# Kernel tuning notes

Measured on AMD Instinct MI355X. Metric: run time of the kernel, lower is better.

## Reference

```python
import jax, jax.numpy as jnp
import numpy as np

MARGIN = 0.2
SCALE = 30.0

def setup_inputs() -> dict:
    key = jax.random.key(0)
    k1, k2 = jax.random.split(key)
    B, D, C = 8192, 512, 100
    embeddings = jax.random.normal(k1, (B, D), dtype=jnp.float32)
    labels = jax.random.randint(k2, (B,), 0, C, dtype=jnp.int64)
    return {"embeddings": embeddings, "labels": labels}

def reference(embeddings, labels):
    # Cosine similarity via one GEMM: normalize rows once, then n @ n.T.
    # (torch F.cosine_similarity uses eps=1e-8 on norms)
    norms = jnp.maximum(jnp.linalg.norm(embeddings, axis=1, keepdims=True), 1e-8)
    n = embeddings / norms                      # [B, D]
    sim = n @ n.T                               # [B, B]
    pos_mask = labels[:, None] == labels[None, :]  # includes diagonal, as in original
    e = jnp.exp(SCALE * (sim - MARGIN))         # [B, B]
    pos_sum = jnp.sum(jnp.where(pos_mask, e, 0.0))
    neg_sum = jnp.sum(jnp.where(pos_mask, 0.0, e))
    loss = jnp.log1p(neg_sum / pos_sum)
    return loss
```

## Files before the change

kernel.cpp:

```cpp
#include <hip/hip_runtime.h>
#include <hip/hip_bf16.h>
#include <math.h>


#define BDIM 8192
#define DDIM 512
#define MARGIN 0.2f
#define SCALE 30.0f

#define BT 256
#define BK 64
#define NKT (DDIM / BK)
#define NT (BDIM / BT)
#define NBLK (NT * (NT + 1) / 2)

typedef __hip_bfloat16 bf16;
using f32x4  = __attribute__((ext_vector_type(4))) float;
using bf16x8 = __attribute__((ext_vector_type(8))) short;
using us8    = __attribute__((ext_vector_type(8))) unsigned short;

#define GLOAD_LDS16(gp, lp)                                                    \
    __builtin_amdgcn_global_load_lds(                                          \
        (const __attribute__((address_space(1))) unsigned int*)(gp),           \
        (__attribute__((address_space(3))) unsigned int*)(lp), 16, 0, 0)

__device__ __forceinline__ unsigned short f2bf(float x) {
    union { bf16 h; unsigned short u; } c;
    c.h = __float2bfloat16(x);
    return c.u;
}

__global__ __launch_bounds__(256)
void norm_rows_kernel(const float* __restrict__ emb, bf16* __restrict__ nout,
                      double* __restrict__ accum, unsigned* __restrict__ ctr) {
    if (blockIdx.x == 0 && threadIdx.x == 0) {
        accum[0] = 0.0; accum[1] = 0.0; *ctr = 0u;
    }
    const int row  = blockIdx.x * 4 + (threadIdx.x >> 6);
    const int lane = threadIdx.x & 63;
    const float4* src = (const float4*)(emb + (size_t)row * DDIM) + lane * 2;
    const float4 a = src[0];
    const float4 b = src[1];
    float ss = a.x * a.x + a.y * a.y + a.z * a.z + a.w * a.w
             + b.x * b.x + b.y * b.y + b.z * b.z + b.w * b.w;
    #pragma unroll
    for (int off = 1; off < 64; off <<= 1) ss += __shfl_xor(ss, off, 64);
    const float inv = 1.0f / fmaxf(sqrtf(ss), 1e-8f);
    float v[8] = { a.x, a.y, a.z, a.w, b.x, b.y, b.z, b.w };
    us8 o;
    #pragma unroll
    for (int i = 0; i < 8; ++i) o[i] = f2bf(v[i] * inv);
    *((us8*)(nout + (size_t)row * DDIM) + lane) = o;
}

__global__ __launch_bounds__(512, 2)
void gemm_loss_kernel(const bf16* __restrict__ nmat,
                      const int* __restrict__ labels,
                      double* __restrict__ accum, unsigned* __restrict__ ctr,
                      float* __restrict__ out) {
    const int l = blockIdx.x;
    auto tri = [](int b) { return ((65 - b) * b) >> 1; };
    int bi = (int)((65.0 - sqrt(4225.0 - 8.0 * (double)l)) * 0.5);
    bi = bi < 0 ? 0 : (bi > 31 ? 31 : bi);
    while (bi > 0 && tri(bi) > l) --bi;
    while (tri(bi + 1) <= l) ++bi;
    const int bj = bi + (l - tri(bi));

    __shared__ short As[2][BT * BK];
    __shared__ short Bs[2][BT * BK];
    __shared__ int lr[BT], lc[BT];
    __shared__ double red[16];

    const int t = threadIdx.x, wid = t >> 6, lane = t & 63;
    if (t < 256) lr[t] = labels[bi * BT + t];
    else         lc[t - 256] = labels[bj * BT + (t - 256)];

    const int wm = wid >> 2;
    const int wn = wid & 3;

    const int srow = wid * 16 + (lane >> 3);
    const int swz8 = ((lane & 7) ^ (lane >> 3)) * 8;
    const bf16* gA = nmat + (size_t)(bi * BT + srow) * DDIM + swz8;
    const bf16* gB = nmat + (size_t)(bj * BT + srow) * DDIM + swz8;
    const int ldsw = wid * 1024;

    #define STAGE_A(buf, kt, h)                                                 \
        do {                                                                    \
            GLOAD_LDS16(gA + (size_t)(h) * 128 * DDIM + (kt) * BK,              \
                        &As[buf][(h) * 8192 + ldsw]);                           \
            GLOAD_LDS16(gA + (size_t)(h) * 128 * DDIM + 8 * DDIM + (kt) * BK,   \
                        &As[buf][(h) * 8192 + ldsw + 512]);                     \
        } while (0)
    #define STAGE_B(buf, kt, h)                                                 \
        do {                                                                    \
            GLOAD_LDS16(gB + (size_t)(h) * 128 * DDIM + (kt) * BK,              \
                        &Bs[buf][(h) * 8192 + ldsw]);                           \
            GLOAD_LDS16(gB + (size_t)(h) * 128 * DDIM + 8 * DDIM + (kt) * BK,   \
                        &Bs[buf][(h) * 8192 + ldsw + 512]);                     \
        } while (0)

    const int arow = (wm * 128 + (lane & 15)) * BK;
    const int brow = (wn * 64 + (lane & 15)) * BK;
    const int chk0 = (((lane >> 4) + 0) ^ (lane & 7)) * 8;
    const int chk1 = (((lane >> 4) + 4) ^ (lane & 7)) * 8;

    f32x4 acc[8][4] = {};

    STAGE_A(0, 0, 0); STAGE_A(0, 0, 1); STAGE_B(0, 0, 0); STAGE_B(0, 0, 1);

    #pragma unroll 2
    for (int kt = 0; kt < NKT; ++kt) {
        const int cur = kt & 1, nxt = cur ^ 1;
        const bool more = (kt + 1 < NKT);
        if (more) {
            STAGE_A(nxt, kt + 1, 0);
            asm volatile("s_waitcnt vmcnt(2)" ::: "memory");
        } else {
            asm volatile("s_waitcnt vmcnt(0)" ::: "memory");
        }
        __builtin_amdgcn_s_barrier();
        asm volatile("" ::: "memory");

        bf16x8 a[4], b[4], a2[4];
        #pragma unroll
        for (int m = 0; m < 4; ++m)
            a[m] = *(const bf16x8*)&As[cur][arow + m * 1024 + chk0];
        #pragma unroll
        for (int n = 0; n < 4; ++n)
            b[n] = *(const bf16x8*)&Bs[cur][brow + n * 1024 + chk0];
        if (more) STAGE_A(nxt, kt + 1, 1);
        __builtin_amdgcn_s_setprio(1);
        #pragma unroll
        for (int m = 0; m < 4; ++m)
            #pragma unroll
            for (int n = 0; n < 4; ++n)
                acc[m][n] = __builtin_amdgcn_mfma_f32_16x16x32_bf16(
                    a[m], b[n], acc[m][n], 0, 0, 0);
        __builtin_amdgcn_s_setprio(0);
        #pragma unroll
        for (int m = 0; m < 4; ++m)
            a2[m] = *(const bf16x8*)&As[cur][arow + (m + 4) * 1024 + chk0];
        if (more) STAGE_B(nxt, kt + 1, 0);
        __builtin_amdgcn_s_setprio(1);
        #pragma unroll
        for (int m = 0; m < 4; ++m)
            #pragma unroll
            for (int n = 0; n < 4; ++n)
                acc[m + 4][n] = __builtin_amdgcn_mfma_f32_16x16x32_bf16(
                    a2[m], b[n], acc[m + 4][n], 0, 0, 0);
        __builtin_amdgcn_s_setprio(0);
        #pragma unroll
        for (int m = 0; m < 4; ++m)
            a[m] = *(const bf16x8*)&As[cur][arow + m * 1024 + chk1];
        #pragma unroll
        for (int n = 0; n < 4; ++n)
            b[n] = *(const bf16x8*)&Bs[cur][brow + n * 1024 + chk1];
        if (more) STAGE_B(nxt, kt + 1, 1);
        __builtin_amdgcn_s_setprio(1);
        #pragma unroll
        for (int m = 0; m < 4; ++m)
            #pragma unroll
            for (int n = 0; n < 4; ++n)
                acc[m][n] = __builtin_amdgcn_mfma_f32_16x16x32_bf16(
                    a[m], b[n], acc[m][n], 0, 0, 0);
        __builtin_amdgcn_s_setprio(0);
        #pragma unroll
        for (int m = 0; m < 4; ++m)
            a2[m] = *(const bf16x8*)&As[cur][arow + (m + 4) * 1024 + chk1];
        asm volatile("s_waitcnt lgkmcnt(0)" ::: "memory");
        __builtin_amdgcn_sched_barrier(0);
        __builtin_amdgcn_s_barrier();
        asm volatile("" ::: "memory");
        __builtin_amdgcn_s_setprio(1);
        #pragma unroll
        for (int m = 0; m < 4; ++m)
            #pragma unroll
            for (int n = 0; n < 4; ++n)
                acc[m + 4][n] = __builtin_amdgcn_mfma_f32_16x16x32_bf16(
                    a2[m], b[n], acc[m + 4][n], 0, 0, 0);
        __builtin_amdgcn_s_setprio(0);
    }
    #undef STAGE_A
    #undef STAGE_B

    float posf = 0.0f, negf = 0.0f;
    const int rbase = wm * 128 + (lane >> 4) * 4;
    const int cbase = wn * 64 + (lane & 15);
    #pragma unroll
    for (int m = 0; m < 8; ++m) {
        #pragma unroll
        for (int n = 0; n < 4; ++n) {
            const int ljv = lc[cbase + n * 16];
            #pragma unroll
            for (int r = 0; r < 4; ++r) {
                const float e = __expf(fmaf(acc[m][n][r], SCALE, -SCALE * MARGIN));
                if (lr[rbase + m * 16 + r] == ljv) posf += e; else negf += e;
            }
        }
    }

    double dp = (double)posf, dn = (double)negf;
    #pragma unroll
    for (int o = 32; o > 0; o >>= 1) {
        dp += __shfl_down(dp, o, 64);
        dn += __shfl_down(dn, o, 64);
    }
    if (lane == 0) { red[wid * 2] = dp; red[wid * 2 + 1] = dn; }
    __syncthreads();
    if (t == 0) {
        const double w = (bi == bj) ? 1.0 : 2.0;
        double p = 0.0, q = 0.0;
        #pragma unroll
        for (int i = 0; i < 8; ++i) { p += red[2 * i]; q += red[2 * i + 1]; }
        atomicAdd(&accum[0], p * w);
        atomicAdd(&accum[1], q * w);
        __threadfence();
        unsigned prev = atomicAdd(ctr, 1u);
        if (prev == NBLK - 1) {
            __threadfence();
            double pp = atomicAdd(&accum[0], 0.0);
            double qq = atomicAdd(&accum[1], 0.0);
            out[0] = (float)log1p(qq / pp);
        }
    }
}

extern "C" void kernel_launch(void* const* d_in, const int* in_sizes, int n_in,
                              void* d_out, int out_size, void* d_ws, size_t ws_size,
                              hipStream_t stream) {
    const float* emb  = (const float*)d_in[0];
    const int* labels = (const int*)d_in[1];
    float* out        = (float*)d_out;

    double* accum = (double*)d_ws;
    unsigned* ctr = (unsigned*)((char*)d_ws + 16);
    bf16* nmat    = (bf16*)((char*)d_ws + 256);

    norm_rows_kernel<<<BDIM / 4, 256, 0, stream>>>(emb, nmat, accum, ctr);
    gemm_loss_kernel<<<NBLK, 512, 0, stream>>>(nmat, labels, accum, ctr, out);
}
```

Baseline: 134.5 us.

## Deepen GEMM pipeline to four-stage BK=32 ring buffer and remap block order

Halves the K tile to 32 and uses a four-slot LDS ring with three tiles prefetched ahead, with vmcnt waits tuned per iteration and a new swizzle for the smaller tile. The loop is fully unrolled, with two barriers per K step. Block indices are also permuted across eight groups, likely to spread tile pairs over XCDs or caches. The aim is to hide global-to-LDS load latency better while keeping the same LDS footprint, at the cost of more barriers per unit of MFMA work and more complex wait accounting.

```diff
diff --git a/kernel.cpp b/kernel.cpp
--- a/kernel.cpp
+++ b/kernel.cpp
@@ -9,7 +9,7 @@
 #define SCALE 30.0f
 
 #define BT 256
-#define BK 64
+#define BK 32
 #define NKT (DDIM / BK)
 #define NT (BDIM / BT)
 #define NBLK (NT * (NT + 1) / 2)
@@ -58,7 +58,8 @@
                       const int* __restrict__ labels,
                       double* __restrict__ accum, unsigned* __restrict__ ctr,
                       float* __restrict__ out) {
-    const int l = blockIdx.x;
+    const int hw = blockIdx.x;
+    const int l = (hw & 7) * (NBLK / 8) + (hw >> 3);
     auto tri = [](int b) { return ((65 - b) * b) >> 1; };
     int bi = (int)((65.0 - sqrt(4225.0 - 8.0 * (double)l)) * 0.5);
     bi = bi < 0 ? 0 : (bi > 31 ? 31 : bi);
@@ -66,69 +67,60 @@
     while (tri(bi + 1) <= l) ++bi;
     const int bj = bi + (l - tri(bi));
 
-    __shared__ short As[2][BT * BK];
-    __shared__ short Bs[2][BT * BK];
+    __shared__ alignas(16) short As[4][BT * BK];
+    __shared__ alignas(16) short Bs[4][BT * BK];
     __shared__ int lr[BT], lc[BT];
     __shared__ double red[16];
 
-    const int t = threadIdx.x, wid = t >> 6, lane = t & 63;
-    if (t < 256) lr[t] = labels[bi * BT + t];
-    else         lc[t - 256] = labels[bj * BT + (t - 256)];
+    const int tix = threadIdx.x, wid = tix >> 6, lane = tix & 63;
+    if (tix < 256) lr[tix] = labels[bi * BT + tix];
+    else           lc[tix - 256] = labels[bj * BT + (tix - 256)];
 
     const int wm = wid >> 2;
     const int wn = wid & 3;
 
-    const int srow = wid * 16 + (lane >> 3);
-    const int swz8 = ((lane & 7) ^ (lane >> 3)) * 8;
-    const bf16* gA = nmat + (size_t)(bi * BT + srow) * DDIM + swz8;
-    const bf16* gB = nmat + (size_t)(bj * BT + srow) * DDIM + swz8;
-    const int ldsw = wid * 1024;
-
-    #define STAGE_A(buf, kt, h)                                                 \
-        do {                                                                    \
-            GLOAD_LDS16(gA + (size_t)(h) * 128 * DDIM + (kt) * BK,              \
-                        &As[buf][(h) * 8192 + ldsw]);                           \
-            GLOAD_LDS16(gA + (size_t)(h) * 128 * DDIM + 8 * DDIM + (kt) * BK,   \
-                        &As[buf][(h) * 8192 + ldsw + 512]);                     \
-        } while (0)
-    #define STAGE_B(buf, kt, h)                                                 \
-        do {                                                                    \
-            GLOAD_LDS16(gB + (size_t)(h) * 128 * DDIM + (kt) * BK,              \
-                        &Bs[buf][(h) * 8192 + ldsw]);                           \
-            GLOAD_LDS16(gB + (size_t)(h) * 128 * DDIM + 8 * DDIM + (kt) * BK,   \
-                        &Bs[buf][(h) * 8192 + ldsw + 512]);                     \
-        } while (0)
-
-    const int arow = (wm * 128 + (lane & 15)) * BK;
-    const int brow = (wn * 64 + (lane & 15)) * BK;
-    const int chk0 = (((lane >> 4) + 0) ^ (lane & 7)) * 8;
-    const int chk1 = (((lane >> 4) + 4) ^ (lane & 7)) * 8;
+    const int srow = wid * 16 + (lane >> 2);
+    const int scol = ((lane & 3) ^ ((lane >> 3) & 3)) * 8;
+    const bf16* gA = nmat + (size_t)(bi * BT + srow) * DDIM + scol;
+    const bf16* gB = nmat + (size_t)(bj * BT + srow) * DDIM + scol;
+    const int ldst = wid * 16 * BK;
+
+    #define STG_A(buf, kt, h)                                                  \
+        GLOAD_LDS16(gA + (size_t)((h) * 128) * DDIM + (kt) * BK,               \
+                    &As[buf][(h) * 128 * BK + ldst])
+    #define STG_B(buf, kt, h)                                                  \
+        GLOAD_LDS16(gB + (size_t)((h) * 128) * DDIM + (kt) * BK,               \
+                    &Bs[buf][(h) * 128 * BK + ldst])
+
+    const int aoff  = (lane & 15) * BK + (((lane >> 4) ^ ((lane >> 1) & 3)) * 8);
+    const int abase = wm * 128 * BK;
+    const int bbase = wn * 64 * BK;
 
     f32x4 acc[8][4] = {};
 
-    STAGE_A(0, 0, 0); STAGE_A(0, 0, 1); STAGE_B(0, 0, 0); STAGE_B(0, 0, 1);
-
-    #pragma unroll 2
-    for (int kt = 0; kt < NKT; ++kt) {
-        const int cur = kt & 1, nxt = cur ^ 1;
-        const bool more = (kt + 1 < NKT);
-        if (more) {
-            STAGE_A(nxt, kt + 1, 0);
-            asm volatile("s_waitcnt vmcnt(2)" ::: "memory");
-        } else {
-            asm volatile("s_waitcnt vmcnt(0)" ::: "memory");
-        }
+    #pragma unroll
+    for (int tt = 0; tt < 3; ++tt) {
+        STG_A(tt, tt, 0); STG_A(tt, tt, 1);
+        STG_B(tt, tt, 0); STG_B(tt, tt, 1);
+    }
+    asm volatile("s_waitcnt vmcnt(8)" ::: "memory");
+    __builtin_amdgcn_s_barrier();
+    asm volatile("" ::: "memory");
+
+    #pragma unroll
+    for (int t = 0; t < NKT; ++t) {
+        const int cur = t & 3, pre = (t + 3) & 3;
+        bf16x8 a[4], b[4];
+        #pragma unroll
+        for (int m = 0; m < 4; ++m)
+            a[m] = *(const bf16x8*)&As[cur][abase + m * (16 * BK) + aoff];
+        #pragma unroll
+        for (int n = 0; n < 4; ++n)
+            b[n] = *(const bf16x8*)&Bs[cur][bbase + n * (16 * BK) + aoff];
+        if (t < NKT - 3) { STG_A(pre, t + 3, 0); STG_A(pre, t + 3, 1); }
         __builtin_amdgcn_s_barrier();
-        asm volatile("" ::: "memory");
-
-        bf16x8 a[4], b[4], a2[4];
-        #pragma unroll
-        for (int m = 0; m < 4; ++m)
-            a[m] = *(const bf16x8*)&As[cur][arow + m * 1024 + chk0];
-        #pragma unroll
-        for (int n = 0; n < 4; ++n)
-            b[n] = *(const bf16x8*)&Bs[cur][brow + n * 1024 + chk0];
-        if (more) STAGE_A(nxt, kt + 1, 1);
+        asm volatile("s_waitcnt lgkmcnt(0)" ::: "memory");
+        __builtin_amdgcn_sched_barrier(0);
         __builtin_amdgcn_s_setprio(1);
         #pragma unroll
         for (int m = 0; m < 4; ++m)
@@ -139,49 +131,25 @@
         __builtin_amdgcn_s_setprio(0);
         #pragma unroll
         for (int m = 0; m < 4; ++m)
-            a2[m] = *(const bf16x8*)&As[cur][arow + (m + 4) * 1024 + chk0];
-        if (more) STAGE_B(nxt, kt + 1, 0);
+            a[m] = *(const bf16x8*)&As[cur][abase + (m + 4) * (16 * BK) + aoff];
+        if (t < NKT - 3) { STG_B(pre, t + 3, 0); STG_B(pre, t + 3, 1); }
+        if (t <= NKT - 4)      { asm volatile("s_waitcnt vmcnt(8)" ::: "memory"); }
+        else if (t == NKT - 3) { asm volatile("s_waitcnt vmcnt(4)" ::: "memory"); }
+        else if (t == NKT - 2) { asm volatile("s_waitcnt vmcnt(0)" ::: "memory"); }
+        __builtin_amdgcn_s_barrier();
+        asm volatile("s_waitcnt lgkmcnt(0)" ::: "memory");
+        __builtin_amdgcn_sched_barrier(0);
         __builtin_amdgcn_s_setprio(1);
         #pragma unroll
         for (int m = 0; m < 4; ++m)
             #pragma unroll
             for (int n = 0; n < 4; ++n)
                 acc[m + 4][n] = __builtin_amdgcn_mfma_f32_16x16x32_bf16(
-                    a2[m], b[n], acc[m + 4][n], 0, 0, 0);
+                    a[m], b[n], acc[m + 4][n], 0, 0, 0);
         __builtin_amdgcn_s_setprio(0);
-        #pragma unroll
-        for (int m = 0; m < 4; ++m)
-            a[m] = *(const bf16x8*)&As[cur][arow + m * 1024 + chk1];
-        #pragma unroll
-        for (int n = 0; n < 4; ++n)
-            b[n] = *(const bf16x8*)&Bs[cur][brow + n * 1024 + chk1];
-        if (more) STAGE_B(nxt, kt + 1, 1);
-        __builtin_amdgcn_s_setprio(1);
-        #pragma unroll
-        for (int m = 0; m < 4; ++m)
-            #pragma unroll
-            for (int n = 0; n < 4; ++n)
-                acc[m][n] = __builtin_amdgcn_mfma_f32_16x16x32_bf16(
-                    a[m], b[n], acc[m][n], 0, 0, 0);
-        __builtin_amdgcn_s_setprio(0);
-        #pragma unroll
-        for (int m = 0; m < 4; ++m)
-            a2[m] = *(const bf16x8*)&As[cur][arow + (m + 4) * 1024 + chk1];
-        asm volatile("s_waitcnt lgkmcnt(0)" ::: "memory");
-        __builtin_amdgcn_sched_barrier(0);
-        __builtin_amdgcn_s_barrier();
-        asm volatile("" ::: "memory");
-        __builtin_amdgcn_s_setprio(1);
-        #pragma unroll
-        for (int m = 0; m < 4; ++m)
-            #pragma unroll
-            for (int n = 0; n < 4; ++n)
-                acc[m + 4][n] = __builtin_amdgcn_mfma_f32_16x16x32_bf16(
-                    a2[m], b[n], acc[m + 4][n], 0, 0, 0);
-        __builtin_amdgcn_s_setprio(0);
-    }
-    #undef STAGE_A
-    #undef STAGE_B
+    }
+    #undef STG_A
+    #undef STG_B
 
     float posf = 0.0f, negf = 0.0f;
     const int rbase = wm * 128 + (lane >> 4) * 4;
@@ -207,7 +175,7 @@
     }
     if (lane == 0) { red[wid * 2] = dp; red[wid * 2 + 1] = dn; }
     __syncthreads();
-    if (t == 0) {
+    if (tix == 0) {
         const double w = (bi == bj) ? 1.0 : 2.0;
         double p = 0.0, q = 0.0;
         #pragma unroll
```

Result: no change. 134.7 us (+0.2%).
